# Optimization experiments

Hardware: AMD Instinct MI355X
Metric: run time of the kernel (lower is better)

Reference implementation:

```python
import jax, jax.numpy as jnp
import numpy as np

EMBED = 512
HEADS = 8
HEAD_DIM = EMBED // HEADS
WINDOW = 256
HALF = WINDOW // 2
B, S = 2, 2048


def setup_inputs() -> dict:
    key = jax.random.key(0)
    kv, kk, kq, kw = jax.random.split(key, 4)
    return {
        "values": jax.random.normal(kv, (B, 1, S, EMBED), dtype=jnp.float32),
        "keys": jax.random.normal(kk, (B, 1, S, EMBED), dtype=jnp.float32),
        "query": jax.random.normal(kq, (B, 1, S, EMBED), dtype=jnp.float32),
        "mask": jnp.ones((B, 1, 1, S), dtype=jnp.int32),
        "fc_w": jax.random.normal(kw, (EMBED, EMBED), dtype=jnp.float32) * (1.0 / np.sqrt(EMBED)),
        "fc_b": jnp.zeros((EMBED,), dtype=jnp.float32),
    }


def reference(values, keys, query, mask, fc_w, fc_b):
    b = query.shape[0]
    s = values.shape[2]
    v = values.reshape(b, s, HEADS, HEAD_DIM)
    k = keys.reshape(b, s, HEADS, HEAD_DIM)
    q = query.reshape(b, s, HEADS, HEAD_DIM)
    scale = jnp.float32(EMBED ** 0.5)

    # global token: query 0 attends to all keys
    gq = q[:, 0:1]  # (b,1,h,d)
    ge = jnp.einsum('bqhd,bkhd->bhqk', gq, k)
    ga = jax.nn.softmax(ge / scale, axis=3)
    gout = jnp.einsum('bhqk,bkhd->bqhd', ga, v)  # (b,1,h,d)

    # sliding-window queries (positions 1..s-1, band centered at local index i)
    wq = q[:, 1:]  # (b, s-1, h, d)
    qw = s - 1
    e = jnp.einsum('bqhd,bkhd->bhqk', wq, k)  # (b,h,qw,s)
    i = jnp.arange(qw)[:, None]
    j = jnp.arange(s)[None, :]
    band = (j >= i - HALF) & (j <= i + HALF)  # (qw, s)
    # faithful to original: out-of-band energies are ZERO (not -inf)
    e = jnp.where(band[None, None], e, jnp.float32(0.0))
    e = jnp.where(mask == 0, jnp.float32(-1e20), e)
    a = jax.nn.softmax(e / scale, axis=3)
    lout = jnp.einsum('bhqk,bkhd->bqhd', a, v)  # (b,qw,h,d)

    out = jnp.concatenate([gout, lout], axis=1).reshape(b, s, HEADS * HEAD_DIM)
    return out @ fc_w.T + fc_b
```

## Files before the change

kernel.cpp:

```cpp
#include <hip/hip_runtime.h>
#include <math.h>

#define EMBED 512
#define HEADS 8
#define HDIM 64
#define SLEN 2048
#define BATCH 2
#define HALFW 128
#define NCHUNK 32
#define INV_SCALE 0.044194173824159216f

typedef short bf16x8 __attribute__((ext_vector_type(8)));
typedef short s16x4  __attribute__((ext_vector_type(4)));
typedef float f32x4  __attribute__((ext_vector_type(4)));

#define MFMA16(a, b, c) __builtin_amdgcn_mfma_f32_16x16x32_bf16(a, b, c, 0, 0, 0)

__device__ __forceinline__ short f2bf(float x) {
    union { float f; unsigned u; } v; v.f = x;
    unsigned r = v.u + 0x7FFFu + ((v.u >> 16) & 1u);
    return (short)(r >> 16);
}

__device__ __forceinline__ int lidx(int row, int seg) {
    return (((seg << 6) + (row ^ seg)) << 3);
}

__device__ __forceinline__ void gll16(const short* g, short* l) {
    __builtin_amdgcn_global_load_lds(
        (const __attribute__((address_space(1))) unsigned int*)g,
        (__attribute__((address_space(3))) unsigned int*)l, 16, 0, 0);
}

__device__ __forceinline__ void stage_chunk(const short* s0, const short* s1,
                                            short* d0, short* d1, int t) {
    int off = t * 8;
    int wb  = (t >> 6) * 512;
    gll16(s0 + off,        d0 + wb);
    gll16(s0 + 2048 + off, d0 + 2048 + wb);
    gll16(s1 + off,        d1 + wb);
    gll16(s1 + 2048 + off, d1 + 2048 + wb);
}

__global__ __launch_bounds__(256) void prepass(
    const float* __restrict__ q, const float* __restrict__ k,
    const float* __restrict__ v, const int* __restrict__ mask,
    const float* __restrict__ fcw,
    short* __restrict__ Kbf, short* __restrict__ Vbf, short* __restrict__ Wbf,
    float* __restrict__ gnum_part, float* __restrict__ gden_part,
    float* __restrict__ vsum_part, float* __restrict__ nval_part) {
    int c = blockIdx.x, h = blockIdx.y, b = blockIdx.z;
    int t = threadIdx.x, w = t >> 6, l = t & 63;

    if (c >= NCHUNK) {
        int nb = b * 4 + (c - NCHUNK);
        size_t base = (size_t)(nb * 8 + h) * 4096;
        #pragma unroll
        for (int p = 0; p < 4; ++p) {
            int idx = p * 256 + t, row = idx >> 4, kg = idx & 15;
            float4 f = *(const float4*)(fcw + (size_t)(nb * 64 + row) * EMBED + h * 64 + kg * 4);
            s16x4 o;
            o[0] = f2bf(f.x); o[1] = f2bf(f.y); o[2] = f2bf(f.z); o[3] = f2bf(f.w);
            *(s16x4*)&Wbf[base + lidx(row, kg >> 1) + (kg & 1) * 4] = o;
        }
        return;
    }

    int j0 = c * 64;
    __shared__ float q0s[HDIM];
    __shared__ float wls[64];
    __shared__ int   m_s[64];
    __shared__ float vbuf[64][68];
    __shared__ float red[4][HDIM];
    __shared__ float redv[4][HDIM];

    if (t < 64) {
        q0s[t] = q[(size_t)b * SLEN * EMBED + h * HDIM + t];
        m_s[t] = mask[b * SLEN + j0 + t];
    }
    __syncthreads();

    size_t fragbase = ((size_t)(b * HEADS + h) * NCHUNK + c) * 4096;

    #pragma unroll
    for (int p = 0; p < 4; ++p) {
        int idx = p * 256 + t, row = idx >> 4, kg = idx & 15;
        float4 f = *(const float4*)(k + ((size_t)b * SLEN + j0 + row) * EMBED + h * HDIM + kg * 4);
        float dot = q0s[kg*4+0]*f.x + q0s[kg*4+1]*f.y + q0s[kg*4+2]*f.z + q0s[kg*4+3]*f.w;
        dot += __shfl_xor(dot, 1, 64);
        dot += __shfl_xor(dot, 2, 64);
        dot += __shfl_xor(dot, 4, 64);
        dot += __shfl_xor(dot, 8, 64);
        if ((t & 15) == 0) wls[row] = __expf(dot * INV_SCALE);
        if (!m_s[row]) f = make_float4(0.f, 0.f, 0.f, 0.f);
        s16x4 o;
        o[0] = f2bf(f.x); o[1] = f2bf(f.y); o[2] = f2bf(f.z); o[3] = f2bf(f.w);
        *(s16x4*)&Kbf[fragbase + lidx(row, kg >> 1) + (kg & 1) * 4] = o;
    }

    #pragma unroll
    for (int p = 0; p < 4; ++p) {
        int idx = p * 256 + t, row = idx >> 4, kg = idx & 15;
        float4 f = *(const float4*)(v + ((size_t)b * SLEN + j0 + row) * EMBED + h * HDIM + kg * 4);
        *(float4*)&vbuf[row][kg * 4] = f;
    }
    __syncthreads();

    float num = 0.f, vs = 0.f;
    #pragma unroll
    for (int jj = 0; jj < 16; ++jj) {
        int jl = w * 16 + jj;
        float vv = vbuf[jl][l];
        num += wls[jl] * vv;
        if (m_s[jl]) vs += vv;
    }
    red[w][l] = num;
    redv[w][l] = vs;

    #pragma unroll
    for (int s = 0; s < 2; ++s) {
        int jseg = w * 2 + s;
        bf16x8 o;
        #pragma unroll
        for (int e = 0; e < 8; ++e) o[e] = f2bf(vbuf[jseg * 8 + e][l]);
        *(bf16x8*)&Vbf[fragbase + lidx(l, jseg)] = o;
    }
    __syncthreads();

    if (w == 0) {
        gnum_part[((size_t)(b * HEADS + h) * NCHUNK + c) * HDIM + l] =
            red[0][l] + red[1][l] + red[2][l] + red[3][l];
        vsum_part[((size_t)b * NCHUNK + c) * EMBED + h * HDIM + l] =
            redv[0][l] + redv[1][l] + redv[2][l] + redv[3][l];
    } else if (w == 1) {
        float s = wls[l];
        #pragma unroll
        for (int off = 32; off > 0; off >>= 1) s += __shfl_xor(s, off, 64);
        if (l == 0) gden_part[(size_t)(b * HEADS + h) * NCHUNK + c] = s;
    } else if (w == 2 && h == 0) {
        float cc = m_s[l] ? 1.f : 0.f;
        #pragma unroll
        for (int off = 32; off > 0; off >>= 1) cc += __shfl_xor(cc, off, 64);
        if (l == 0) nval_part[b * NCHUNK + c] = cc;
    }
}

__global__ __launch_bounds__(256) void windowed_attn_v6(
    const float* __restrict__ q, const float* __restrict__ k,
    const float* __restrict__ v, const int* __restrict__ mask,
    const short* __restrict__ Kbf, const short* __restrict__ Vbf,
    const float* __restrict__ gnum_part, const float* __restrict__ gden_part,
    const float* __restrict__ vsum_part, const float* __restrict__ nval_part,
    short* __restrict__ Abf) {
    int tile = blockIdx.x, h = blockIdx.y, b = blockIdx.z;
    int r0 = tile * 64;
    int t = threadIdx.x, w = t >> 6, l = t & 63;
    int lg = l >> 4, lr = l & 15;

    __shared__ __align__(16) short k_s[2][4096];
    __shared__ __align__(16) short v_s[2][4096];
    __shared__ __align__(16) short wT_s[4][16][72];
    __shared__ float rsum[64];
    __shared__ float vred[4][64];
    __shared__ float gred[4][64];
    __shared__ float nv_s, gd_s;

    size_t hb = (size_t)(b * HEADS + h) * NCHUNK;
    int bh = b * HEADS + h;

    int c0 = tile - 2; if (c0 < 0) c0 = 0;
    int c1 = tile + 2; if (c1 > NCHUNK - 1) c1 = NCHUNK - 1;

    stage_chunk(Kbf + (hb + c0) * 4096, Vbf + (hb + c0) * 4096,
                &k_s[0][0], &v_s[0][0], t);

    const float* qrow = q + ((size_t)b * SLEN + r0 + w * 16 + lr) * EMBED + h * HDIM;
    float4 a0 = *(const float4*)(qrow + lg * 8);
    float4 a1 = *(const float4*)(qrow + lg * 8 + 4);
    float4 a2 = *(const float4*)(qrow + 32 + lg * 8);
    float4 a3 = *(const float4*)(qrow + 32 + lg * 8 + 4);
    bf16x8 qb0, qb1;
    qb0[0] = f2bf(a0.x); qb0[1] = f2bf(a0.y); qb0[2] = f2bf(a0.z); qb0[3] = f2bf(a0.w);
    qb0[4] = f2bf(a1.x); qb0[5] = f2bf(a1.y); qb0[6] = f2bf(a1.z); qb0[7] = f2bf(a1.w);
    qb1[0] = f2bf(a2.x); qb1[1] = f2bf(a2.y); qb1[2] = f2bf(a2.z); qb1[3] = f2bf(a2.w);
    qb1[4] = f2bf(a3.x); qb1[5] = f2bf(a3.y); qb1[6] = f2bf(a3.z); qb1[7] = f2bf(a3.w);

    {
        float vp = 0.f;
        #pragma unroll
        for (int cc = 0; cc < 8; ++cc)
            vp += vsum_part[((size_t)b * NCHUNK + w * 8 + cc) * EMBED + h * HDIM + l];
        vred[w][l] = vp;
        if (w == 0) {
            float nvv = (l < NCHUNK) ? nval_part[b * NCHUNK + l] : 0.f;
            #pragma unroll
            for (int off = 32; off > 0; off >>= 1) nvv += __shfl_xor(nvv, off, 64);
            if (l == 0) nv_s = nvv;
        }
        if (tile == 0) {
            float gp = 0.f;
            #pragma unroll
            for (int cc = 0; cc < 8; ++cc)
                gp += gnum_part[((size_t)bh * NCHUNK + w * 8 + cc) * HDIM + l];
            gred[w][l] = gp;
            if (w == 1) {
                float gdd = (l < NCHUNK) ? gden_part[(size_t)bh * NCHUNK + l] : 0.f;
                #pragma unroll
                for (int off = 32; off > 0; off >>= 1) gdd += __shfl_xor(gdd, off, 64);
                if (l == 0) gd_s = gdd;
            }
        }
    }

    int center = r0 + w * 16 + lr - 1;
    int lo = center - HALFW, hi = center + HALFW;

    f32x4 pv[4];
    #pragma unroll
    for (int dt = 0; dt < 4; ++dt) pv[dt] = (f32x4){0.f, 0.f, 0.f, 0.f};
    float dacc = 0.f;
    int cur = 0;

    asm volatile("s_waitcnt vmcnt(0)" ::: "memory");
    __syncthreads();

    for (int c = c0; c <= c1; ++c) {
        if (c < c1)
            stage_chunk(Kbf + (hb + c + 1) * 4096, Vbf + (hb + c + 1) * 4096,
                        &k_s[cur ^ 1][0], &v_s[cur ^ 1][0], t);
        int jc = c * 64;

        #pragma unroll
        for (int jt = 0; jt < 4; ++jt) {
            bf16x8 ka0 = *(const bf16x8*)&k_s[cur][lidx(jt * 16 + lr, lg)];
            bf16x8 ka1 = *(const bf16x8*)&k_s[cur][lidx(jt * 16 + lr, 4 + lg)];
            f32x4 sT = (f32x4){0.f, 0.f, 0.f, 0.f};
            sT = MFMA16(ka0, qb0, sT);
            sT = MFMA16(ka1, qb1, sT);
            int jbase = jc + jt * 16 + lg * 4;
            s16x4 wq;
            #pragma unroll
            for (int r = 0; r < 4; ++r) {
                int j = jbase + r;
                float wgt = (j >= lo && j <= hi) ? (__expf(sT[r] * INV_SCALE) - 1.f) : 0.f;
                dacc += wgt;
                wq[r] = f2bf(wgt);
            }
            *(s16x4*)&wT_s[w][lr][jt * 16 + lg * 4] = wq;
        }

        bf16x8 wa0 = *(const bf16x8*)&wT_s[w][lr][lg * 8];
        bf16x8 wa1 = *(const bf16x8*)&wT_s[w][lr][32 + lg * 8];
        #pragma unroll
        for (int dt = 0; dt < 4; ++dt) {
            bf16x8 va0 = *(const bf16x8*)&v_s[cur][lidx(dt * 16 + lr, lg)];
            bf16x8 va1 = *(const bf16x8*)&v_s[cur][lidx(dt * 16 + lr, 4 + lg)];
            pv[dt] = MFMA16(wa0, va0, pv[dt]);
            pv[dt] = MFMA16(wa1, va1, pv[dt]);
        }

        asm volatile("s_waitcnt vmcnt(0)" ::: "memory");
        __syncthreads();
        cur ^= 1;
    }

    float wfix = 0.f;
    int jx = r0 - 129;
    if (w == 0 && jx >= 0) {
        float qv = q[((size_t)b * SLEN + r0) * EMBED + h * HDIM + l];
        float kv = k[((size_t)b * SLEN + jx) * EMBED + h * HDIM + l];
        float dd = qv * kv;
        #pragma unroll
        for (int off = 32; off > 0; off >>= 1) dd += __shfl_xor(dd, off, 64);
        if (mask[b * SLEN + jx] != 0) wfix = __expf(dd * INV_SCALE) - 1.f;
        if (lg == 0) {
            #pragma unroll
            for (int dt = 0; dt < 4; ++dt)
                pv[dt][0] += wfix * v[((size_t)b * SLEN + jx) * EMBED + h * HDIM + dt * 16 + lr];
        }
    }

    dacc += __shfl_xor(dacc, 16, 64);
    dacc += __shfl_xor(dacc, 32, 64);
    if (lg == 0) rsum[w * 16 + lr] = dacc + ((w == 0 && lr == 0) ? wfix : 0.f);
    __syncthreads();

    float nv = nv_s;
    float invden[4];
    #pragma unroll
    for (int r = 0; r < 4; ++r)
        invden[r] = 1.f / (nv + rsum[w * 16 + lg * 4 + r]);

    short* Atile = Abf + ((size_t)(b * NCHUNK + tile) * 8 + h) * 4096;
    #pragma unroll
    for (int dt = 0; dt < 4; ++dt) {
        int d = dt * 16 + lr;
        float vs = vred[0][d] + vred[1][d] + vred[2][d] + vred[3][d];
        #pragma unroll
        for (int r = 0; r < 4; ++r) {
            int row_local = w * 16 + lg * 4 + r;
            float o;
            if (tile == 0 && row_local == 0)
                o = (gred[0][d] + gred[1][d] + gred[2][d] + gred[3][d]) / gd_s;
            else
                o = (pv[dt][r] + vs) * invden[r];
            Atile[lidx(row_local, d >> 3) + (d & 7)] = f2bf(o);
        }
    }
}

__global__ __launch_bounds__(256) void fc_gemm_v3(
    const short* __restrict__ Abf, const short* __restrict__ Wbf,
    const float* __restrict__ bias, float* __restrict__ C) {
    int bm = blockIdx.x;
    int nb = blockIdx.y;
    int t = threadIdx.x, w = t >> 6, l = t & 63;
    int lg = l >> 4, lr = l & 15;
    int wr = w >> 1, wc = w & 1;

    __shared__ __align__(16) short a_s[2][4096];
    __shared__ __align__(16) short b_s[2][4096];

    f32x4 acc[2][2];
    #pragma unroll
    for (int mt = 0; mt < 2; ++mt)
        #pragma unroll
        for (int nt = 0; nt < 2; ++nt) acc[mt][nt] = (f32x4){0.f, 0.f, 0.f, 0.f};

    stage_chunk(Abf + (size_t)(bm * 8 + 0) * 4096, Wbf + (size_t)(nb * 8 + 0) * 4096,
                &a_s[0][0], &b_s[0][0], t);
    asm volatile("s_waitcnt vmcnt(0)" ::: "memory");
    __syncthreads();
    int cur = 0;

    for (int kt = 0; kt < 8; ++kt) {
        if (kt < 7)
            stage_chunk(Abf + (size_t)(bm * 8 + kt + 1) * 4096,
                        Wbf + (size_t)(nb * 8 + kt + 1) * 4096,
                        &a_s[cur ^ 1][0], &b_s[cur ^ 1][0], t);

        bf16x8 af[2][2], bf_[2][2];
        #pragma unroll
        for (int mt = 0; mt < 2; ++mt) {
            af[mt][0] = *(const bf16x8*)&a_s[cur][lidx(wr * 32 + mt * 16 + lr, lg)];
            af[mt][1] = *(const bf16x8*)&a_s[cur][lidx(wr * 32 + mt * 16 + lr, 4 + lg)];
        }
        #pragma unroll
        for (int nt = 0; nt < 2; ++nt) {
            bf_[nt][0] = *(const bf16x8*)&b_s[cur][lidx(wc * 32 + nt * 16 + lr, lg)];
            bf_[nt][1] = *(const bf16x8*)&b_s[cur][lidx(wc * 32 + nt * 16 + lr, 4 + lg)];
        }
        #pragma unroll
        for (int mt = 0; mt < 2; ++mt)
            #pragma unroll
            for (int nt = 0; nt < 2; ++nt) {
                acc[mt][nt] = MFMA16(af[mt][0], bf_[nt][0], acc[mt][nt]);
                acc[mt][nt] = MFMA16(af[mt][1], bf_[nt][1], acc[mt][nt]);
            }

        asm volatile("s_waitcnt vmcnt(0)" ::: "memory");
        __syncthreads();
        cur ^= 1;
    }

    #pragma unroll
    for (int mt = 0; mt < 2; ++mt)
        #pragma unroll
        for (int nt = 0; nt < 2; ++nt) {
            int n = nb * 64 + wc * 32 + nt * 16 + lr;
            float bb = bias[n];
            #pragma unroll
            for (int reg = 0; reg < 4; ++reg) {
                int m = bm * 64 + wr * 32 + mt * 16 + lg * 4 + reg;
                C[(size_t)m * 512 + n] = acc[mt][nt][reg] + bb;
            }
        }
}

extern "C" void kernel_launch(void* const* d_in, const int* in_sizes, int n_in,
                              void* d_out, int out_size, void* d_ws, size_t ws_size,
                              hipStream_t stream) {
    const float* values = (const float*)d_in[0];
    const float* keys   = (const float*)d_in[1];
    const float* query  = (const float*)d_in[2];
    const int*   maskp  = (const int*)d_in[3];
    const float* fc_w   = (const float*)d_in[4];
    const float* fc_b   = (const float*)d_in[5];
    float* out = (float*)d_out;

    short* Abf = (short*)d_ws;
    short* Wbf = Abf + (size_t)BATCH * SLEN * EMBED;
    short* Kbf = Wbf + (size_t)EMBED * EMBED;
    short* Vbf = Kbf + (size_t)BATCH * HEADS * NCHUNK * 4096;
    float* vsum_part = (float*)(Vbf + (size_t)BATCH * HEADS * NCHUNK * 4096);
    float* gnum_part = vsum_part + (size_t)BATCH * NCHUNK * EMBED;
    float* gden_part = gnum_part + (size_t)BATCH * HEADS * NCHUNK * HDIM;
    float* nval_part = gden_part + (size_t)BATCH * HEADS * NCHUNK;

    prepass<<<dim3(NCHUNK + 4, HEADS, BATCH), 256, 0, stream>>>(
        query, keys, values, maskp, fc_w, Kbf, Vbf, Wbf,
        gnum_part, gden_part, vsum_part, nval_part);
    windowed_attn_v6<<<dim3(NCHUNK, HEADS, BATCH), 256, 0, stream>>>(
        query, keys, values, maskp, Kbf, Vbf,
        gnum_part, gden_part, vsum_part, nval_part, Abf);
    fc_gemm_v3<<<dim3(BATCH * NCHUNK, EMBED / 64), 256, 0, stream>>>(
        Abf, Wbf, fc_b, out);
}
```

Baseline: 36.82 us.

## Deepen prefetch pipelines in attention and FC GEMM kernels

The attention kernel moves from double to triple buffering of the K/V chunks. It prefetches two chunks ahead and uses partial vmcnt waits, so loads can stay in flight across iterations. The FC GEMM now issues the loads for all 8 A tiles up front, double-buffers the W tiles, and waits with partial vmcnt counts instead of draining every iteration. This raises LDS use (the GEMM needs 80KB of shared memory), which may lower occupancy. Correctness also relies on the vmcnt counts matching the number of loads each staging step issues.

```diff
diff --git a/kernel.cpp b/kernel.cpp
--- a/kernel.cpp
+++ b/kernel.cpp
@@ -145,7 +145,7 @@
     }
 }
 
-__global__ __launch_bounds__(256) void windowed_attn_v6(
+__global__ __launch_bounds__(256) void windowed_attn_v7(
     const float* __restrict__ q, const float* __restrict__ k,
     const float* __restrict__ v, const int* __restrict__ mask,
     const short* __restrict__ Kbf, const short* __restrict__ Vbf,
@@ -157,8 +157,8 @@
     int t = threadIdx.x, w = t >> 6, l = t & 63;
     int lg = l >> 4, lr = l & 15;
 
-    __shared__ __align__(16) short k_s[2][4096];
-    __shared__ __align__(16) short v_s[2][4096];
+    __shared__ __align__(16) short k_s[3][4096];
+    __shared__ __align__(16) short v_s[3][4096];
     __shared__ __align__(16) short wT_s[4][16][72];
     __shared__ float rsum[64];
     __shared__ float vred[4][64];
@@ -212,6 +212,9 @@
         }
     }
 
+    stage_chunk(Kbf + (hb + c0 + 1) * 4096, Vbf + (hb + c0 + 1) * 4096,
+                &k_s[1][0], &v_s[1][0], t);
+
     int center = r0 + w * 16 + lr - 1;
     int lo = center - HALFW, hi = center + HALFW;
 
@@ -219,21 +222,18 @@
     #pragma unroll
     for (int dt = 0; dt < 4; ++dt) pv[dt] = (f32x4){0.f, 0.f, 0.f, 0.f};
     float dacc = 0.f;
-    int cur = 0;
-
-    asm volatile("s_waitcnt vmcnt(0)" ::: "memory");
-    __syncthreads();
-
+
+    int bi = 0;
     for (int c = c0; c <= c1; ++c) {
-        if (c < c1)
-            stage_chunk(Kbf + (hb + c + 1) * 4096, Vbf + (hb + c + 1) * 4096,
-                        &k_s[cur ^ 1][0], &v_s[cur ^ 1][0], t);
+        if (c < c1) { asm volatile("s_waitcnt vmcnt(4)" ::: "memory"); }
+        else        { asm volatile("s_waitcnt vmcnt(0)" ::: "memory"); }
+        __syncthreads();
+
         int jc = c * 64;
-
         #pragma unroll
         for (int jt = 0; jt < 4; ++jt) {
-            bf16x8 ka0 = *(const bf16x8*)&k_s[cur][lidx(jt * 16 + lr, lg)];
-            bf16x8 ka1 = *(const bf16x8*)&k_s[cur][lidx(jt * 16 + lr, 4 + lg)];
+            bf16x8 ka0 = *(const bf16x8*)&k_s[bi][lidx(jt * 16 + lr, lg)];
+            bf16x8 ka1 = *(const bf16x8*)&k_s[bi][lidx(jt * 16 + lr, 4 + lg)];
             f32x4 sT = (f32x4){0.f, 0.f, 0.f, 0.f};
             sT = MFMA16(ka0, qb0, sT);
             sT = MFMA16(ka1, qb1, sT);
@@ -253,15 +253,18 @@
         bf16x8 wa1 = *(const bf16x8*)&wT_s[w][lr][32 + lg * 8];
         #pragma unroll
         for (int dt = 0; dt < 4; ++dt) {
-            bf16x8 va0 = *(const bf16x8*)&v_s[cur][lidx(dt * 16 + lr, lg)];
-            bf16x8 va1 = *(const bf16x8*)&v_s[cur][lidx(dt * 16 + lr, 4 + lg)];
+            bf16x8 va0 = *(const bf16x8*)&v_s[bi][lidx(dt * 16 + lr, lg)];
+            bf16x8 va1 = *(const bf16x8*)&v_s[bi][lidx(dt * 16 + lr, 4 + lg)];
             pv[dt] = MFMA16(wa0, va0, pv[dt]);
             pv[dt] = MFMA16(wa1, va1, pv[dt]);
         }
 
-        asm volatile("s_waitcnt vmcnt(0)" ::: "memory");
-        __syncthreads();
-        cur ^= 1;
+        if (c + 2 <= c1) {
+            int bn = bi + 2; if (bn >= 3) bn -= 3;
+            stage_chunk(Kbf + (hb + c + 2) * 4096, Vbf + (hb + c + 2) * 4096,
+                        &k_s[bn][0], &v_s[bn][0], t);
+        }
+        ++bi; if (bi == 3) bi = 0;
     }
 
     float wfix = 0.f;
@@ -309,7 +312,7 @@
     }
 }
 
-__global__ __launch_bounds__(256) void fc_gemm_v3(
+__global__ __launch_bounds__(256) void fc_gemm_v4(
     const short* __restrict__ Abf, const short* __restrict__ Wbf,
     const float* __restrict__ bias, float* __restrict__ C) {
     int bm = blockIdx.x;
@@ -318,8 +321,26 @@
     int lg = l >> 4, lr = l & 15;
     int wr = w >> 1, wc = w & 1;
 
-    __shared__ __align__(16) short a_s[2][4096];
-    __shared__ __align__(16) short b_s[2][4096];
+    __shared__ __align__(16) short a_s[8][4096];
+    __shared__ __align__(16) short w_s[2][4096];
+
+    int off = t * 8;
+    int wb  = (t >> 6) * 512;
+
+    #pragma unroll
+    for (int kt = 0; kt < 8; ++kt) {
+        const short* as = Abf + (size_t)(bm * 8 + kt) * 4096;
+        gll16(as + off,        &a_s[kt][wb]);
+        gll16(as + 2048 + off, &a_s[kt][2048 + wb]);
+    }
+    {
+        const short* ws0 = Wbf + (size_t)(nb * 8 + 0) * 4096;
+        gll16(ws0 + off,        &w_s[0][wb]);
+        gll16(ws0 + 2048 + off, &w_s[0][2048 + wb]);
+        const short* ws1 = Wbf + (size_t)(nb * 8 + 1) * 4096;
+        gll16(ws1 + off,        &w_s[1][wb]);
+        gll16(ws1 + 2048 + off, &w_s[1][2048 + wb]);
+    }
 
     f32x4 acc[2][2];
     #pragma unroll
@@ -327,28 +348,22 @@
         #pragma unroll
         for (int nt = 0; nt < 2; ++nt) acc[mt][nt] = (f32x4){0.f, 0.f, 0.f, 0.f};
 
-    stage_chunk(Abf + (size_t)(bm * 8 + 0) * 4096, Wbf + (size_t)(nb * 8 + 0) * 4096,
-                &a_s[0][0], &b_s[0][0], t);
-    asm volatile("s_waitcnt vmcnt(0)" ::: "memory");
-    __syncthreads();
-    int cur = 0;
-
     for (int kt = 0; kt < 8; ++kt) {
-        if (kt < 7)
-            stage_chunk(Abf + (size_t)(bm * 8 + kt + 1) * 4096,
-                        Wbf + (size_t)(nb * 8 + kt + 1) * 4096,
-                        &a_s[cur ^ 1][0], &b_s[cur ^ 1][0], t);
+        if (kt < 7) { asm volatile("s_waitcnt vmcnt(2)" ::: "memory"); }
+        else        { asm volatile("s_waitcnt vmcnt(0)" ::: "memory"); }
+        __syncthreads();
 
         bf16x8 af[2][2], bf_[2][2];
         #pragma unroll
         for (int mt = 0; mt < 2; ++mt) {
-            af[mt][0] = *(const bf16x8*)&a_s[cur][lidx(wr * 32 + mt * 16 + lr, lg)];
-            af[mt][1] = *(const bf16x8*)&a_s[cur][lidx(wr * 32 + mt * 16 + lr, 4 + lg)];
-        }
+            af[mt][0] = *(const bf16x8*)&a_s[kt][lidx(wr * 32 + mt * 16 + lr, lg)];
+            af[mt][1] = *(const bf16x8*)&a_s[kt][lidx(wr * 32 + mt * 16 + lr, 4 + lg)];
+        }
+        int wbuf = kt & 1;
         #pragma unroll
         for (int nt = 0; nt < 2; ++nt) {
-            bf_[nt][0] = *(const bf16x8*)&b_s[cur][lidx(wc * 32 + nt * 16 + lr, lg)];
-            bf_[nt][1] = *(const bf16x8*)&b_s[cur][lidx(wc * 32 + nt * 16 + lr, 4 + lg)];
+            bf_[nt][0] = *(const bf16x8*)&w_s[wbuf][lidx(wc * 32 + nt * 16 + lr, lg)];
+            bf_[nt][1] = *(const bf16x8*)&w_s[wbuf][lidx(wc * 32 + nt * 16 + lr, 4 + lg)];
         }
         #pragma unroll
         for (int mt = 0; mt < 2; ++mt)
@@ -358,9 +373,12 @@
                 acc[mt][nt] = MFMA16(af[mt][1], bf_[nt][1], acc[mt][nt]);
             }
 
-        asm volatile("s_waitcnt vmcnt(0)" ::: "memory");
         __syncthreads();
-        cur ^= 1;
+        if (kt + 2 <= 7) {
+            const short* ws = Wbf + (size_t)(nb * 8 + kt + 2) * 4096;
+            gll16(ws + off,        &w_s[wbuf][wb]);
+            gll16(ws + 2048 + off, &w_s[wbuf][2048 + wb]);
+        }
     }
 
     #pragma unroll
@@ -400,9 +418,9 @@
     prepass<<<dim3(NCHUNK + 4, HEADS, BATCH), 256, 0, stream>>>(
         query, keys, values, maskp, fc_w, Kbf, Vbf, Wbf,
         gnum_part, gden_part, vsum_part, nval_part);
-    windowed_attn_v6<<<dim3(NCHUNK, HEADS, BATCH), 256, 0, stream>>>(
+    windowed_attn_v7<<<dim3(NCHUNK, HEADS, BATCH), 256, 0, stream>>>(
         query, keys, values, maskp, Kbf, Vbf,
         gnum_part, gden_part, vsum_part, nval_part, Abf);
-    fc_gemm_v3<<<dim3(BATCH * NCHUNK, EMBED / 64), 256, 0, stream>>>(
+    fc_gemm_v4<<<dim3(BATCH * NCHUNK, EMBED / 64), 256, 0, stream>>>(
         Abf, Wbf, fc_b, out);
 }
```

New measurement: 34.91 us. -5.2%, faster.
